# Kernel tuning notes

Hardware: AMD Instinct MI355X
Metric: run time of the kernel (lower is better)

Reference implementation:

```python
import jax, jax.numpy as jnp
import numpy as np

SCORE_THRESH = 0.05  # score_thresh arg of interaction_inference_single_image


def setup_inputs() -> dict:
    key = jax.random.key(0)
    ks = jax.random.split(key, 6)
    R, K = 262144, 117
    return {
        "person_boxes": jax.random.uniform(ks[0], (R, 4), dtype=jnp.float32) * 512.0,
        "object_boxes": jax.random.uniform(ks[1], (R, 4), dtype=jnp.float32) * 512.0,
        "person_box_scores": jax.random.uniform(ks[2], (R,), dtype=jnp.float32),
        "object_box_scores": jax.random.uniform(ks[3], (R,), dtype=jnp.float32),
        "object_box_classes": jax.random.randint(ks[4], (R, 1), 0, 80, dtype=jnp.int32),
        "hoi_scores": jax.random.uniform(ks[5], (R, K), dtype=jnp.float32),
        "topk_per_image": 100,
    }


def reference(person_boxes, object_boxes, person_box_scores, object_box_scores,
              object_box_classes, hoi_scores, topk_per_image):
    # scores[r, k] = hoi_scores[r, k] * person_score[r] * object_score[r]
    R, K = hoi_scores.shape
    box_scores = person_box_scores * object_box_scores          # (R,)
    scores = hoi_scores * box_scores[:, None]                    # (R, K)

    # Fused threshold + top-k: entries failing the threshold are pushed to -inf
    # so they can never enter the top-k; `valid` marks real detections.
    flat = scores.reshape(-1)                                    # (R*K,)
    masked = jnp.where(flat > SCORE_THRESH, flat, -jnp.inf)
    top_vals, top_idx = jax.lax.top_k(masked, topk_per_image)    # sorted descending
    valid = top_vals > SCORE_THRESH                              # (topk,) bool

    pair_idx = top_idx // K                                      # filter_inds[:, 0]
    action_classes = top_idx % K                                 # filter_inds[:, 1]

    out_scores = jnp.where(valid, top_vals, 0.0)
    out_person_boxes = person_boxes[pair_idx]                    # (topk, 4)
    out_object_boxes = object_boxes[pair_idx]                    # (topk, 4)
    out_object_classes = object_box_classes[pair_idx, 0]         # (topk,)
    return (out_scores, out_person_boxes, out_object_boxes,
            out_object_classes, action_classes, valid)
```

## Files before the change

### kernel.cpp

```cpp
#include <hip/hip_runtime.h>


#define NB        576
#define BIN_BASE  15692
#define WLO       500
#define WN        80
#define VLO       0.75f
#define G_REL     538
#define FCAP      2048
#define NREP      32
#define REPS      96
#define UNROLL    8
#define THRESH    0.05f
#define NEG_INF   __int_as_float(0xFF800000)

__device__ __forceinline__ int bin_of(float s) {
  int b = (int)(__float_as_uint(s) >> 16) - BIN_BASE;
  return b > (NB - 1) ? (NB - 1) : b;
}


template <int KC>
__global__ __launch_bounds__(256) void k_main(
    const float4* __restrict__ hoi4, const float* __restrict__ ps,
    const float* __restrict__ os, int N4, int N, int Kc,
    int* __restrict__ ctrl, int* __restrict__ rep,
    float* __restrict__ cand_v, int* __restrict__ cand_i, int cap) {
  __shared__ int lh[WN];
  if (threadIdx.x < WN) lh[threadIdx.x] = 0;
  __syncthreads();

  const int k = KC ? KC : Kc;
  const int TT = gridDim.x * blockDim.x;
  const int tid = blockIdx.x * blockDim.x + threadIdx.x;

  auto process = [&](int t, const float4& h) {
    int i0 = 4 * t;
    int q = i0 / k;
    int rem = i0 - q * k;
    float bsa = ps[q] * os[q];
    int qb = (rem + 3 >= k) ? q + 1 : q;
    float bsb = ps[qb] * os[qb];
    float vals[4] = {h.x, h.y, h.z, h.w};
#pragma unroll
    for (int j = 0; j < 4; ++j) {
      float s = vals[j] * ((rem + j >= k) ? bsb : bsa);
      if (s > VLO) {
        int b = bin_of(s);
        atomicAdd(&lh[b - WLO], 1);
        if (b >= G_REL) {
          int slot = atomicAdd(&ctrl[0], 1);
          if (slot < cap) { cand_v[slot] = s; cand_i[slot] = i0 + j; }
        }
      }
    }
  };

  for (int t0 = tid; t0 < N4; t0 += UNROLL * TT) {
    float4 h[UNROLL];
#pragma unroll
    for (int j = 0; j < UNROLL; ++j) {
      int t = t0 + j * TT;
      h[j] = hoi4[t < N4 ? t : t0];
    }
#pragma unroll
    for (int j = 0; j < UNROLL; ++j) {
      int t = t0 + j * TT;
      if (t < N4) process(t, h[j]);
    }
  }
  if (blockIdx.x == 0) {
    const float* hoi = (const float*)hoi4;
    for (int i = N4 * 4 + threadIdx.x; i < N; i += blockDim.x) {
      int q = i / k;
      float s = hoi[i] * (ps[q] * os[q]);
      if (s > VLO) {
        int b = bin_of(s);
        atomicAdd(&lh[b - WLO], 1);
        if (b >= G_REL) {
          int slot = atomicAdd(&ctrl[0], 1);
          if (slot < cap) { cand_v[slot] = s; cand_i[slot] = i; }
        }
      }
    }
  }
  __syncthreads();
  if (threadIdx.x < WN) {
    int c = lh[threadIdx.x];
    if (c) atomicAdd(&rep[(blockIdx.x & (NREP - 1)) * REPS + threadIdx.x], c);
  }
}

__global__ __launch_bounds__(1024) void k_post(
    const float* __restrict__ hoi, const float* __restrict__ ps,
    const float* __restrict__ os, const float4* __restrict__ pbox,
    const float4* __restrict__ obox, const int* __restrict__ ocls,
    int N, int Kc, const int* __restrict__ ctrl, const int* __restrict__ rep,
    const float* __restrict__ cand_v, const int* __restrict__ cand_i,
    int cap, float* __restrict__ out, int topk) {
  __shared__ int wh[NB];
  __shared__ float sv[FCAP];
  __shared__ int si[FCAP];
  __shared__ int s_T, s_n, s_cnt, s_mode;

  if (threadIdx.x < WN) {
    int sum = 0;
#pragma unroll
    for (int r = 0; r < NREP; ++r) sum += rep[r * REPS + threadIdx.x];
    wh[threadIdx.x] = sum;
  }
  __syncthreads();
  if (threadIdx.x == 0) {
    int cum = 0, T = -1;
    for (int b = WN - 1; b >= 0; --b) {
      cum += wh[b];
      if (T < 0 && cum >= topk) T = b + WLO;
    }
    int cnt = ctrl[0];
    s_mode = (T >= G_REL && cnt <= cap) ? 1 : 0;
    s_T = T;
    s_n = cnt > cap ? cap : cnt;
    s_cnt = 0;
  }
  __syncthreads();

  if (s_mode) {
    const int T = s_T, n = s_n;
    for (int t = threadIdx.x; t < n; t += blockDim.x) {
      float v = cand_v[t];
      if (bin_of(v) >= T) {
        int slot = atomicAdd(&s_cnt, 1);
        if (slot < FCAP) { sv[slot] = v; si[slot] = cand_i[t]; }
      }
    }
  } else {
    for (int b = threadIdx.x; b < NB; b += blockDim.x) wh[b] = 0;
    __syncthreads();
    for (int i = threadIdx.x; i < N; i += blockDim.x) {
      int q = i / Kc;
      float s = hoi[i] * (ps[q] * os[q]);
      if (s > THRESH) atomicAdd(&wh[bin_of(s)], 1);
    }
    __syncthreads();
    if (threadIdx.x == 0) {
      int cum = 0, T = 0;
      for (int b = NB - 1; b >= 0; --b) {
        cum += wh[b];
        if (cum >= topk) { T = b; break; }
      }
      s_T = T;
    }
    __syncthreads();
    const int T = s_T;
    for (int i = threadIdx.x; i < N; i += blockDim.x) {
      int q = i / Kc;
      float s = hoi[i] * (ps[q] * os[q]);
      if (s > THRESH && bin_of(s) >= T) {
        int slot = atomicAdd(&s_cnt, 1);
        if (slot < FCAP) { sv[slot] = s; si[slot] = i; }
      }
    }
  }
  __syncthreads();

  int m = s_cnt > FCAP ? FCAP : s_cnt;
  int P = 128;
  while (P < m) P <<= 1;
  for (int t = m + threadIdx.x; t < P; t += blockDim.x) {
    sv[t] = NEG_INF;
    si[t] = 0x7FFFFFFF;
  }
  for (int kk = 2; kk <= P; kk <<= 1) {
    for (int j = kk >> 1; j > 0; j >>= 1) {
      __syncthreads();
      for (int i = threadIdx.x; i < P; i += blockDim.x) {
        int l = i ^ j;
        if (l > i) {
          float vi = sv[i], vl = sv[l];
          int ii = si[i], il = si[l];
          bool before = (vi > vl) || (vi == vl && ii < il);
          if (((i & kk) == 0) != before) {
            sv[i] = vl; sv[l] = vi; si[i] = il; si[l] = ii;
          }
        }
      }
    }
  }
  __syncthreads();

  if ((int)threadIdx.x < topk) {
    int o = threadIdx.x;
    float v = sv[o];
    int idx = si[o];
    bool valid = (idx != 0x7FFFFFFF) && (v > THRESH);
    int safe = valid ? idx : 0;
    int pair = safe / Kc;
    int act = safe - pair * Kc;
    float4 pb = pbox[pair];
    float4 ob = obox[pair];
    out[o] = valid ? v : 0.0f;
    float* pdst = out + topk + 4 * o;
    pdst[0] = pb.x; pdst[1] = pb.y; pdst[2] = pb.z; pdst[3] = pb.w;
    float* odst = out + 5 * topk + 4 * o;
    odst[0] = ob.x; odst[1] = ob.y; odst[2] = ob.z; odst[3] = ob.w;
    out[9 * topk + o] = (float)ocls[pair];
    out[10 * topk + o] = (float)act;
    out[11 * topk + o] = valid ? 1.0f : 0.0f;
  }
}

extern "C" void kernel_launch(void* const* d_in, const int* in_sizes, int n_in,
                              void* d_out, int out_size, void* d_ws, size_t ws_size,
                              hipStream_t stream) {
  const float* pbox = (const float*)d_in[0];
  const float* obox = (const float*)d_in[1];
  const float* ps   = (const float*)d_in[2];
  const float* os   = (const float*)d_in[3];
  const int*   ocls = (const int*)d_in[4];
  const float* hoi  = (const float*)d_in[5];
  float* out = (float*)d_out;

  const int R    = in_sizes[2];
  const int N    = in_sizes[5];
  const int Kc   = N / R;
  const int topk = out_size / 12;

  int* ctrl = (int*)d_ws;
  int* rep  = (int*)((char*)d_ws + 256);
  float* cand_v = (float*)((char*)d_ws + 12544);
  size_t cand_budget = (ws_size > 12544) ? (ws_size - 12544) / 8 : 1024;
  int cap = cand_budget > 8192 ? 8192 : (int)cand_budget;
  int* cand_i = (int*)((char*)d_ws + 12544 + (size_t)cap * sizeof(float));

  hipMemsetAsync(d_ws, 0, 12544, stream);

  const int N4 = N / 4;
  if (Kc == 117) {
    k_main<117><<<2048, 256, 0, stream>>>((const float4*)hoi, ps, os, N4, N,
                                          Kc, ctrl, rep, cand_v, cand_i, cap);
  } else {
    k_main<0><<<2048, 256, 0, stream>>>((const float4*)hoi, ps, os, N4, N, Kc,
                                        ctrl, rep, cand_v, cand_i, cap);
  }
  k_post<<<1, 1024, 0, stream>>>(hoi, ps, os, (const float4*)pbox,
                                 (const float4*)obox, ocls, N, Kc, ctrl, rep,
                                 cand_v, cand_i, cap, out, topk);
}
```

Baseline: 222.0 us.

## Partition main scan by row chunks and stage box-score products in shared memory

```diff
diff --git a/kernel.cpp b/kernel.cpp
--- a/kernel.cpp
+++ b/kernel.cpp
@@ -10,6 +10,7 @@
 #define FCAP      2048
 #define NREP      32
 #define REPS      96
+#define RPB       128
 #define UNROLL    8
 #define THRESH    0.05f
 #define NEG_INF   __int_as_float(0xFF800000)
@@ -22,68 +23,79 @@
 
 template <int KC>
 __global__ __launch_bounds__(256) void k_main(
-    const float4* __restrict__ hoi4, const float* __restrict__ ps,
-    const float* __restrict__ os, int N4, int N, int Kc,
+    const float* __restrict__ hoi, const float* __restrict__ ps,
+    const float* __restrict__ os, int R, int Kc,
     int* __restrict__ ctrl, int* __restrict__ rep,
     float* __restrict__ cand_v, int* __restrict__ cand_i, int cap) {
+  __shared__ float lbsf[RPB + 1];
+  __shared__ float2 lbs2[RPB];
   __shared__ int lh[WN];
+
+  const int k = KC ? KC : Kc;
+  const int r0 = blockIdx.x * RPB;
+  const int nr = (R - r0) < RPB ? (R - r0) : RPB;
+
   if (threadIdx.x < WN) lh[threadIdx.x] = 0;
-  __syncthreads();
-
-  const int k = KC ? KC : Kc;
-  const int TT = gridDim.x * blockDim.x;
-  const int tid = blockIdx.x * blockDim.x + threadIdx.x;
+  for (int r = threadIdx.x; r < nr; r += blockDim.x)
+    lbsf[r] = ps[r0 + r] * os[r0 + r];
+  if (threadIdx.x == 0) lbsf[nr] = 0.0f;
+  __syncthreads();
+  for (int r = threadIdx.x; r < nr; r += blockDim.x)
+    lbs2[r] = make_float2(lbsf[r], lbsf[r + 1]);
+  __syncthreads();
+
+  const int base = r0 * k;
+  const int nfloat = nr * k;
+  const int nf4 = nfloat >> 2;
+  const float4* c4 = (const float4*)(hoi + base);
 
   auto process = [&](int t, const float4& h) {
     int i0 = 4 * t;
     int q = i0 / k;
     int rem = i0 - q * k;
-    float bsa = ps[q] * os[q];
-    int qb = (rem + 3 >= k) ? q + 1 : q;
-    float bsb = ps[qb] * os[qb];
+    float2 b2 = lbs2[q];
     float vals[4] = {h.x, h.y, h.z, h.w};
 #pragma unroll
     for (int j = 0; j < 4; ++j) {
-      float s = vals[j] * ((rem + j >= k) ? bsb : bsa);
+      float s = vals[j] * ((rem + j >= k) ? b2.y : b2.x);
       if (s > VLO) {
         int b = bin_of(s);
         atomicAdd(&lh[b - WLO], 1);
         if (b >= G_REL) {
           int slot = atomicAdd(&ctrl[0], 1);
-          if (slot < cap) { cand_v[slot] = s; cand_i[slot] = i0 + j; }
+          if (slot < cap) { cand_v[slot] = s; cand_i[slot] = base + i0 + j; }
         }
       }
     }
   };
 
-  for (int t0 = tid; t0 < N4; t0 += UNROLL * TT) {
+  const int BD = blockDim.x;
+  for (int t0 = threadIdx.x; t0 < nf4; t0 += UNROLL * BD) {
     float4 h[UNROLL];
 #pragma unroll
     for (int j = 0; j < UNROLL; ++j) {
-      int t = t0 + j * TT;
-      h[j] = hoi4[t < N4 ? t : t0];
+      int t = t0 + j * BD;
+      h[j] = c4[t < nf4 ? t : t0];
     }
 #pragma unroll
     for (int j = 0; j < UNROLL; ++j) {
-      int t = t0 + j * TT;
-      if (t < N4) process(t, h[j]);
-    }
-  }
-  if (blockIdx.x == 0) {
-    const float* hoi = (const float*)hoi4;
-    for (int i = N4 * 4 + threadIdx.x; i < N; i += blockDim.x) {
-      int q = i / k;
-      float s = hoi[i] * (ps[q] * os[q]);
-      if (s > VLO) {
-        int b = bin_of(s);
-        atomicAdd(&lh[b - WLO], 1);
-        if (b >= G_REL) {
-          int slot = atomicAdd(&ctrl[0], 1);
-          if (slot < cap) { cand_v[slot] = s; cand_i[slot] = i; }
-        }
-      }
-    }
-  }
+      int t = t0 + j * BD;
+      if (t < nf4) process(t, h[j]);
+    }
+  }
+  for (int i = (nf4 << 2) + threadIdx.x; i < nfloat; i += BD) {
+    int q = i / k;
+    float s = hoi[base + i] * lbsf[q];
+    if (s > VLO) {
+      int b = bin_of(s);
+      atomicAdd(&lh[b - WLO], 1);
+      if (b >= G_REL) {
+        int slot = atomicAdd(&ctrl[0], 1);
+        if (slot < cap) { cand_v[slot] = s; cand_i[slot] = base + i; }
+      }
+    }
+  }
+
   __syncthreads();
   if (threadIdx.x < WN) {
     int c = lh[threadIdx.x];
@@ -234,13 +246,13 @@
 
   hipMemsetAsync(d_ws, 0, 12544, stream);
 
-  const int N4 = N / 4;
+  const int nblocks = (R + RPB - 1) / RPB;
   if (Kc == 117) {
-    k_main<117><<<2048, 256, 0, stream>>>((const float4*)hoi, ps, os, N4, N,
-                                          Kc, ctrl, rep, cand_v, cand_i, cap);
+    k_main<117><<<nblocks, 256, 0, stream>>>(hoi, ps, os, R, Kc, ctrl, rep,
+                                             cand_v, cand_i, cap);
   } else {
-    k_main<0><<<2048, 256, 0, stream>>>((const float4*)hoi, ps, os, N4, N, Kc,
-                                        ctrl, rep, cand_v, cand_i, cap);
+    k_main<0><<<nblocks, 256, 0, stream>>>(hoi, ps, os, R, Kc, ctrl, rep,
+                                           cand_v, cand_i, cap);
   }
   k_post<<<1, 1024, 0, stream>>>(hoi, ps, os, (const float4*)pbox,
                                  (const float4*)obox, ocls, N, Kc, ctrl, rep,
```

Result: faster. 215.3 us (-3.0%).
